# Kernel optimization log

Measured on AMD Instinct MI355X. Metric: run time of the kernel, lower is better.

The kernel has to match this reference:

```python
import jax, jax.numpy as jnp
import numpy as np

N = 300000      # total points
B = 4           # scenes
C_IN = 64
C_OUT = 128
GRID = 0.5      # voxel size
M = 128         # per-axis voxel index bound (10m / 0.5m = 20 << 128); key fits int32
EPS = 1e-5      # BatchNorm eps


def setup_inputs() -> dict:
    key = jax.random.key(0)
    k1, k2, k3 = jax.random.split(key, 3)
    coord = jax.random.uniform(k1, (N, 3), jnp.float32) * 10.0
    feat = jax.random.normal(k2, (N, C_IN), jnp.float32)
    offset = jnp.array([N // 4, N // 2, 3 * N // 4, N], jnp.int32)  # cumulative counts
    W = jax.random.normal(k3, (C_IN, C_OUT), jnp.float32) * 0.05    # fc weight (no bias)
    gamma = jnp.ones((C_OUT,), jnp.float32)
    beta = jnp.zeros((C_OUT,), jnp.float32)
    return {"coord": coord, "feat": feat, "offset": offset, "W": W, "gamma": gamma, "beta": beta}


def reference(coord, feat, offset, W, gamma, beta):
    n = coord.shape[0]
    # offset2batch: point i belongs to scene searchsorted(offset, i, 'right')
    batch = jnp.searchsorted(offset, jnp.arange(n, dtype=offset.dtype), side='right')
    # fc -> BatchNorm1d (training-mode batch stats, biased var) -> ReLU
    x = feat @ W                                    # [n, C_OUT]
    mean = x.mean(axis=0)
    var = x.var(axis=0)
    x = jax.nn.relu(gamma * (x - mean) * jax.lax.rsqrt(var + EPS) + beta)
    # start = per-scene min coordinate (segment_csr min)
    start = jax.ops.segment_min(coord, batch, num_segments=B)      # [B, 3]
    # voxel_grid: integer voxel index per point, hashed injectively with batch id
    v = jnp.floor((coord - start[batch]) / GRID).astype(jnp.int32)  # [n, 3]
    vkey = ((batch.astype(jnp.int32) * M + v[:, 0]) * M + v[:, 1]) * M + v[:, 2]
    # unique(sorted) with inverse/counts; padded to n for static shapes
    uniq, cluster, counts = jnp.unique(vkey, return_inverse=True, return_counts=True,
                                       size=n, fill_value=-1)
    cluster = cluster.reshape(-1)                   # [n] cluster id per point
    # segment mean of coords, segment max of features (padded segments -> 0)
    cnt = jnp.maximum(counts, 1).astype(coord.dtype)
    coord_out = jax.ops.segment_sum(coord, cluster, num_segments=n) / cnt[:, None]
    fmax = jax.ops.segment_max(x, cluster, num_segments=n)
    feat_out = jnp.where(counts[:, None] > 0, fmax, jnp.zeros((), x.dtype))
    # batch id of each cluster (clusters never cross scenes)
    batch_out = jax.ops.segment_min(batch, cluster, num_segments=n)
    return coord_out, feat_out, cluster, counts, batch_out
```

## Files before the change

### kernel.cpp

```cpp
#include <hip/hip_runtime.h>
#include <stdint.h>

#define CIN   64
#define COUT  128
#define EPSB  1e-5f
#define NWORDS2 4096
#define MAXNC 32768
#define STRD  68

typedef short bf16x8 __attribute__((ext_vector_type(8)));
typedef float f32x4  __attribute__((ext_vector_type(4)));

__device__ __forceinline__ int batch_of(int i, const int* __restrict__ off, int B) {
    int b = 0;
    for (int j = 0; j < B - 1; ++j) b += (i >= off[j]) ? 1 : 0;
    return b;
}

__device__ __forceinline__ unsigned enc(float x) {
    unsigned b = __float_as_uint(x);
    return (b & 0x80000000u) ? ~b : (b | 0x80000000u);
}
__device__ __forceinline__ float dec(unsigned u) {
    unsigned b = (u & 0x80000000u) ? (u ^ 0x80000000u) : ~u;
    return __uint_as_float(b);
}

__device__ __forceinline__ unsigned short rne_bf16(float f) {
    unsigned u = __float_as_uint(f);
    unsigned r = u + 0x7FFFu + ((u >> 16) & 1u);
    return (unsigned short)(r >> 16);
}

__global__ void k_init(float* __restrict__ coordOut, float* __restrict__ batchOut, int n,
                       unsigned* __restrict__ pooledU, int* __restrict__ countsWs,
                       unsigned* __restrict__ flags, int* __restrict__ sceneMin, int nScene,
                       const float* __restrict__ W, unsigned short* __restrict__ Wb)
{
    long i = (long)blockIdx.x * blockDim.x + threadIdx.x;
    long stride = (long)gridDim.x * blockDim.x;
    for (long t = i; t < 3L * n; t += stride) coordOut[t] = 0.f;
    for (long t = i; t < n; t += stride) batchOut[t] = 2147483648.0f;
    for (long t = i; t < (long)MAXNC * COUT; t += stride) pooledU[t] = 0u;
    for (long t = i; t < MAXNC; t += stride) countsWs[t] = 0;
    for (long t = i; t < NWORDS2; t += stride) flags[t] = 0u;
    for (long t = i; t < nScene; t += stride) sceneMin[t] = 0x7F800000;
    for (long t = i; t < 32 * 64 * 8; t += stride) {
        int fragIdx = (int)(t >> 9);
        int r = (int)(t & 511);
        int lane = r >> 3, j = r & 7;
        int s  = fragIdx & 1;
        int kt = (fragIdx >> 1) & 1;
        int nt = fragIdx >> 2;
        int k  = kt * 32 + (lane >> 4) * 8 + j;
        int nc = nt * 16 + (lane & 15);
        float w = W[k * COUT + nc];
        unsigned short hi = rne_bf16(w);
        if (s == 0) Wb[t] = hi;
        else {
            float hf = __uint_as_float(((unsigned)hi) << 16);
            Wb[t] = rne_bf16(w - hf);
        }
    }
}

__global__ void k_scene_min(const float* __restrict__ coord, const int* __restrict__ off,
                            int n, int B, int* __restrict__ sceneMin)
{
    __shared__ int smin[12];
    if (threadIdx.x < 3 * B) smin[threadIdx.x] = 0x7F800000;
    __syncthreads();
    int t = blockIdx.x * blockDim.x + threadIdx.x;
    if (t < n) {
        int b = batch_of(t, off, B);
        for (int d = 0; d < 3; ++d)
            atomicMin(&smin[b * 3 + d], __float_as_int(coord[t * 3 + d]));
    }
    __syncthreads();
    if (threadIdx.x < 3 * B) atomicMin(&sceneMin[threadIdx.x], smin[threadIdx.x]);
}

__device__ __forceinline__ int vox_key(const float* __restrict__ coord, int t, int b,
                                       const int* __restrict__ sceneMin)
{
    int key = b;
    for (int d = 0; d < 3; ++d) {
        float s = __int_as_float(sceneMin[b * 3 + d]);
        int v = (int)floorf((coord[t * 3 + d] - s) * 2.0f);
        key = (key << 5) + v;
    }
    return key;
}

__global__ void k_vkey(const float* __restrict__ coord, const int* __restrict__ off,
                       int n, int B, const int* __restrict__ sceneMin,
                       unsigned* __restrict__ flags)
{
    int t = blockIdx.x * blockDim.x + threadIdx.x;
    if (t >= n) return;
    int key = vox_key(coord, t, batch_of(t, off, B), sceneMin);
    atomicOr(&flags[key >> 5], 1u << (key & 31));
}

__global__ void k_scan1(const unsigned* __restrict__ flags,
                        unsigned* __restrict__ wordPrefix, int* __restrict__ dNC)
{
    __shared__ unsigned s[1024];
    int t = threadIdx.x;
    unsigned loc[4]; unsigned sum = 0;
    #pragma unroll
    for (int e = 0; e < 4; ++e) { loc[e] = (unsigned)__popc(flags[4 * t + e]); sum += loc[e]; }
    s[t] = sum;
    __syncthreads();
    for (int d = 1; d < 1024; d <<= 1) {
        unsigned a = (t >= d) ? s[t - d] : 0u;
        __syncthreads();
        s[t] += a;
        __syncthreads();
    }
    unsigned run = s[t] - sum;
    #pragma unroll
    for (int e = 0; e < 4; ++e) { wordPrefix[4 * t + e] = run; run += loc[e]; }
    if (t == 1023) *dNC = (int)s[1023];
}

__global__ void k_cluster(const float* __restrict__ coord, const int* __restrict__ off,
                          int n, int B, const int* __restrict__ sceneMin,
                          const unsigned* __restrict__ flags, const unsigned* __restrict__ wordPrefix,
                          float* __restrict__ clusterOut,
                          int* __restrict__ countsWs, float* __restrict__ batchOut,
                          float* __restrict__ coordOut)
{
    int t = blockIdx.x * blockDim.x + threadIdx.x;
    if (t >= n) return;
    int b = batch_of(t, off, B);
    float c0 = coord[t * 3 + 0], c1 = coord[t * 3 + 1], c2 = coord[t * 3 + 2];
    int key = b;
    key = (key << 5) + (int)floorf((c0 - __int_as_float(sceneMin[b * 3 + 0])) * 2.0f);
    key = (key << 5) + (int)floorf((c1 - __int_as_float(sceneMin[b * 3 + 1])) * 2.0f);
    key = (key << 5) + (int)floorf((c2 - __int_as_float(sceneMin[b * 3 + 2])) * 2.0f);
    int w = key >> 5, bit = key & 31;
    int c = (int)wordPrefix[w] + __popc(flags[w] & ((1u << bit) - 1u));
    clusterOut[t] = (float)c;
    atomicAdd(&countsWs[c], 1);
    batchOut[c] = (float)b;
    atomicAdd(&coordOut[c * 3 + 0], c0);
    atomicAdd(&coordOut[c * 3 + 1], c1);
    atomicAdd(&coordOut[c * 3 + 2], c2);
}

__global__ void k_scan2(const int* __restrict__ counts, int* __restrict__ cursor)
{
    __shared__ int s[1024];
    int t = threadIdx.x;
    int base = t * 32;
    int loc[32]; int sum = 0;
    #pragma unroll
    for (int e = 0; e < 32; ++e) { loc[e] = counts[base + e]; sum += loc[e]; }
    s[t] = sum;
    __syncthreads();
    for (int d = 1; d < 1024; d <<= 1) {
        int a = (t >= d) ? s[t - d] : 0;
        __syncthreads();
        s[t] += a;
        __syncthreads();
    }
    int run = s[t] - sum;
    #pragma unroll
    for (int e = 0; e < 32; ++e) { cursor[base + e] = run; run += loc[e]; }
}

__global__ void k_scatter(const float* __restrict__ clusterOut, int n,
                          int* __restrict__ cursor, int* __restrict__ perm,
                          int* __restrict__ sortedCid)
{
    int t = blockIdx.x * blockDim.x + threadIdx.x;
    if (t >= n) return;
    int c = (int)clusterOut[t];
    int pos = atomicAdd(&cursor[c], 1);
    perm[pos] = t;
    sortedCid[pos] = c;
}

__global__ __launch_bounds__(256, 2) void k_fused(
    const float* __restrict__ feat, const unsigned short* __restrict__ Wb,
    const int* __restrict__ perm, const int* __restrict__ sortedCid,
    int n, int nWin, int gFused,
    unsigned* __restrict__ pooledU, float* __restrict__ partials)
{
    __shared__ float lds[4][64 * STRD];
    __shared__ float accS[256];
    const int tid = threadIdx.x, wave = tid >> 6, lane = tid & 63;
    accS[tid] = 0.f;
    __syncthreads();

    const int wid = blockIdx.x * 4 + wave;
    const int q = lane >> 4, c16 = lane & 15;

    if (wid < nWin) {
        const int base = wid * 64;
        const int nvalid = min(64, n - base);
        const int pv = (lane < nvalid) ? perm[base + lane] : 0;
        const int cv = (lane < nvalid) ? sortedCid[base + lane] : -1;
        float* st = lds[wave];

        int prevc = __shfl_up(cv, 1, 64);
        unsigned long long bmask = __ballot(lane > 0 && lane < nvalid && cv != prevc);

        for (int i0 = 0; i0 < 64; i0 += 4) {
            int idx = i0 + q % 4;
            idx = i0 + q;
            int p = __shfl(pv, idx, 64);
            float4 v = make_float4(0.f, 0.f, 0.f, 0.f);
            if (idx < nvalid)
                v = ((const float4*)(feat + (size_t)p * CIN))[c16];
            *(float4*)&st[idx * STRD + c16 * 4] = v;
        }

        bf16x8 ahi[4][2], alo[4][2];
        #pragma unroll
        for (int mt = 0; mt < 4; ++mt) {
            #pragma unroll
            for (int kt = 0; kt < 2; ++kt) {
                int m = mt * 16 + c16;
                int k0 = kt * 32 + q * 8;
                float4 fa = *(const float4*)&st[m * STRD + k0];
                float4 fb = *(const float4*)&st[m * STRD + k0 + 4];
                float tmp[8] = { fa.x, fa.y, fa.z, fa.w, fb.x, fb.y, fb.z, fb.w };
                bf16x8 h8, l8;
                #pragma unroll
                for (int j = 0; j < 8; ++j) {
                    unsigned short h = rne_bf16(tmp[j]);
                    float hf = __uint_as_float(((unsigned)h) << 16);
                    h8[j] = (short)h;
                    l8[j] = (short)rne_bf16(tmp[j] - hf);
                }
                ahi[mt][kt] = h8;
                alo[mt][kt] = l8;
            }
        }

        for (int h = 0; h < 2; ++h) {
            bf16x8 bh[4][2], bl[4][2];
            #pragma unroll
            for (int nt2 = 0; nt2 < 4; ++nt2)
                #pragma unroll
                for (int kt = 0; kt < 2; ++kt) {
                    int fi = h * 16 + (nt2 * 2 + kt) * 2;
                    bh[nt2][kt] = *(const bf16x8*)(Wb + ((size_t)fi << 9) + (lane << 3));
                    bl[nt2][kt] = *(const bf16x8*)(Wb + ((size_t)(fi + 1) << 9) + (lane << 3));
                }
            #pragma unroll
            for (int mt = 0; mt < 4; ++mt) {
                #pragma unroll
                for (int nt2 = 0; nt2 < 4; ++nt2) {
                    f32x4 c = {0.f, 0.f, 0.f, 0.f};
                    #pragma unroll
                    for (int kt = 0; kt < 2; ++kt) {
                        c = __builtin_amdgcn_mfma_f32_16x16x32_bf16(alo[mt][kt], bh[nt2][kt], c, 0, 0, 0);
                        c = __builtin_amdgcn_mfma_f32_16x16x32_bf16(ahi[mt][kt], bl[nt2][kt], c, 0, 0, 0);
                        c = __builtin_amdgcn_mfma_f32_16x16x32_bf16(ahi[mt][kt], bh[nt2][kt], c, 0, 0, 0);
                    }
                    int col = nt2 * 16 + c16;
                    int row0 = mt * 16 + q * 4;
                    *(float4*)&st[col * STRD + row0] = make_float4(c[0], c[1], c[2], c[3]);
                }
            }
            float runM = -INFINITY, s1 = 0.f, s2 = 0.f;
            int runStart = 0;
            for (int ip = 0; ip < 16; ++ip) {
                if (ip * 4 >= nvalid) break;
                float4 v = *(const float4*)&st[lane * STRD + ip * 4];
                #pragma unroll
                for (int e = 0; e < 4; ++e) {
                    int i = ip * 4 + e;
                    if (i < nvalid) {
                        if (i > 0 && ((bmask >> i) & 1ull)) {
                            int cid = __shfl(cv, i - 1, 64);
                            unsigned* pb = pooledU + (size_t)cid * COUT + h * 64 + lane;
                            if (runStart == 0) atomicMax(pb, enc(runM));
                            else               *pb = enc(runM);
                            runStart = i;
                            runM = -INFINITY;
                        }
                        float x = (e == 0) ? v.x : (e == 1) ? v.y : (e == 2) ? v.z : v.w;
                        runM = fmaxf(runM, x);
                        s1 += x;
                        s2 = fmaf(x, x, s2);
                    }
                }
            }
            int cidL = __shfl(cv, nvalid - 1, 64);
            atomicMax(pooledU + (size_t)cidL * COUT + h * 64 + lane, enc(runM));
            atomicAdd(&accS[h * 64 + lane],       s1);
            atomicAdd(&accS[128 + h * 64 + lane], s2);
        }
    }

    __syncthreads();
    partials[(size_t)tid * gFused + blockIdx.x] = accS[tid];
}

__global__ void k_redbn(const float* __restrict__ partials, int gFused,
                        const float* __restrict__ gamma, const float* __restrict__ beta,
                        int n, float* __restrict__ scaleShift)
{
    __shared__ float red[512];
    const int j = blockIdx.x;
    const float* colS = partials + (size_t)j * gFused;
    const float* colQ = partials + (size_t)(j + 128) * gFused;
    float s = 0.f, q = 0.f;
    for (int b = threadIdx.x; b < gFused; b += 256) { s += colS[b]; q += colQ[b]; }
    red[threadIdx.x] = s;
    red[256 + threadIdx.x] = q;
    __syncthreads();
    for (int st = 128; st; st >>= 1) {
        if (threadIdx.x < st) {
            red[threadIdx.x] += red[threadIdx.x + st];
            red[256 + threadIdx.x] += red[256 + threadIdx.x + st];
        }
        __syncthreads();
    }
    if (threadIdx.x == 0) {
        float mean = red[0] / (float)n;
        float var  = red[256] / (float)n - mean * mean;
        var = fmaxf(var, 0.f);
        float inv = rsqrtf(var + EPSB);
        float sc = gamma[j] * inv;
        scaleShift[j]        = sc;
        scaleShift[COUT + j] = beta[j] - mean * sc;
    }
}

__global__ void k_final(float* __restrict__ featOut, const unsigned* __restrict__ pooledU,
                        const int* __restrict__ dNC, const float* __restrict__ scaleShift,
                        long featN4, int n,
                        float* __restrict__ coordOut, float* __restrict__ countsOut,
                        const int* __restrict__ countsWs)
{
    long i = (long)blockIdx.x * blockDim.x + threadIdx.x;
    long stride = (long)gridDim.x * blockDim.x;
    long act4 = (long)(*dNC) * (COUT / 4);
    float4* out4 = (float4*)featOut;
    const uint4* p4 = (const uint4*)pooledU;
    for (long idx = i; idx < featN4; idx += stride) {
        float4 v = make_float4(0.f, 0.f, 0.f, 0.f);
        if (idx < act4) {
            int j = (int)((idx * 4) & (COUT - 1));
            uint4 u = p4[idx];
            v.x = fmaxf(fmaf(scaleShift[j + 0], dec(u.x), scaleShift[COUT + j + 0]), 0.f);
            v.y = fmaxf(fmaf(scaleShift[j + 1], dec(u.y), scaleShift[COUT + j + 1]), 0.f);
            v.z = fmaxf(fmaf(scaleShift[j + 2], dec(u.z), scaleShift[COUT + j + 2]), 0.f);
            v.w = fmaxf(fmaf(scaleShift[j + 3], dec(u.w), scaleShift[COUT + j + 3]), 0.f);
        }
        out4[idx] = v;
    }
    for (long t = i; t < n; t += stride) {
        int cnt = (t < MAXNC) ? countsWs[t] : 0;
        if (cnt > 0) {
            float inv = 1.f / (float)cnt;
            coordOut[3 * t + 0] *= inv;
            coordOut[3 * t + 1] *= inv;
            coordOut[3 * t + 2] *= inv;
        }
        countsOut[t] = (float)cnt;
    }
}

extern "C" void kernel_launch(void* const* d_in, const int* in_sizes, int n_in,
                              void* d_out, int out_size, void* d_ws, size_t ws_size,
                              hipStream_t stream)
{
    const float* coord = (const float*)d_in[0];
    const float* feat  = (const float*)d_in[1];
    const int*   off   = (const int*)d_in[2];
    const float* W     = (const float*)d_in[3];
    const float* gamma = (const float*)d_in[4];
    const float* beta  = (const float*)d_in[5];
    const int n = in_sizes[0] / 3;
    const int B = in_sizes[2];

    float* out        = (float*)d_out;
    float* coordOut   = out;
    float* featOut    = out + (long)n * 3;
    float* clusterOut = featOut + (long)n * COUT;
    float* countsOut  = clusterOut + n;
    float* batchOut   = countsOut + n;

    char* wsp = (char*)d_ws;
    auto alloc = [&](size_t bytes) -> char* {
        char* p = wsp;
        wsp += (bytes + 255) & ~(size_t)255;
        return p;
    };
    unsigned* flags      = (unsigned*)alloc(NWORDS2 * 4);
    unsigned* wordPrefix = (unsigned*)alloc(NWORDS2 * 4);
    int*      countsWs   = (int*)alloc(MAXNC * 4);
    int*      perm       = (int*)alloc((size_t)n * 4);
    int*      sortedCid  = (int*)alloc((size_t)n * 4);
    int*      cursor     = (int*)alloc(MAXNC * 4);
    unsigned* pooledU    = (unsigned*)alloc((size_t)MAXNC * COUT * 4);
    unsigned short* Wb   = (unsigned short*)alloc(32 * 64 * 8 * 2);
    float*    scaleShift = (float*)alloc(2 * COUT * 4);
    int*      sceneMin   = (int*)alloc(3 * B * 4);
    int*      dNC        = (int*)alloc(4);

    const int nWin = (n + 63) / 64;
    const int gFused = (nWin + 3) / 4;
    float*    partials   = (float*)alloc((size_t)gFused * 256 * 4);

    const long featN4 = (long)n * COUT / 4;
    const int nb = (n + 255) / 256;

    k_init<<<nb, 256, 0, stream>>>(coordOut, batchOut, n, pooledU, countsWs,
                                   flags, sceneMin, 3 * B, W, Wb);
    k_scene_min<<<nb, 256, 0, stream>>>(coord, off, n, B, sceneMin);
    k_vkey<<<nb, 256, 0, stream>>>(coord, off, n, B, sceneMin, flags);
    k_scan1<<<1, 1024, 0, stream>>>(flags, wordPrefix, dNC);
    k_cluster<<<nb, 256, 0, stream>>>(coord, off, n, B, sceneMin, flags, wordPrefix,
                                      clusterOut, countsWs, batchOut, coordOut);
    k_scan2<<<1, 1024, 0, stream>>>(countsWs, cursor);
    k_scatter<<<nb, 256, 0, stream>>>(clusterOut, n, cursor, perm, sortedCid);
    k_fused<<<gFused, 256, 0, stream>>>(feat, Wb, perm, sortedCid, n, nWin, gFused,
                                        pooledU, partials);
    k_redbn<<<128, 256, 0, stream>>>(partials, gFused, gamma, beta, n, scaleShift);
    k_final<<<2048, 256, 0, stream>>>(featOut, pooledU, dNC, scaleShift, featN4, n,
                                      coordOut, countsOut, countsWs);
}
```

Before: 443.6 us.

## Cache voxel keys, move coord pooling into sorted fused kernel, shuffle-based scans

The voxel key computed in k_vkey is now stored in a workspace and reused by k_cluster, so coords and scene minima are not re-read there. The batch id is taken from the key bits. The per-point coord atomics in k_cluster are removed. Coord sums are instead accumulated per run of equal cluster ids inside the sorted fused kernel, using plain stores for runs fully inside a window and atomics only at window edges. Both single-block scans switch from LDS Hillis-Steele with many barriers to wave shuffles plus a small cross-wave step. The costs are an extra n-int workspace and a serial per-window loop over 64 points in the fused kernel.

```diff
diff --git a/kernel.cpp b/kernel.cpp
--- a/kernel.cpp
+++ b/kernel.cpp
@@ -80,92 +80,101 @@
     if (threadIdx.x < 3 * B) atomicMin(&sceneMin[threadIdx.x], smin[threadIdx.x]);
 }
 
-__device__ __forceinline__ int vox_key(const float* __restrict__ coord, int t, int b,
-                                       const int* __restrict__ sceneMin)
-{
+__global__ void k_vkey(const float* __restrict__ coord, const int* __restrict__ off,
+                       int n, int B, const int* __restrict__ sceneMin,
+                       int* __restrict__ vkeyWs, unsigned* __restrict__ flags)
+{
+    int t = blockIdx.x * blockDim.x + threadIdx.x;
+    if (t >= n) return;
+    int b = batch_of(t, off, B);
     int key = b;
+    #pragma unroll
     for (int d = 0; d < 3; ++d) {
         float s = __int_as_float(sceneMin[b * 3 + d]);
         int v = (int)floorf((coord[t * 3 + d] - s) * 2.0f);
         key = (key << 5) + v;
     }
-    return key;
-}
-
-__global__ void k_vkey(const float* __restrict__ coord, const int* __restrict__ off,
-                       int n, int B, const int* __restrict__ sceneMin,
-                       unsigned* __restrict__ flags)
+    vkeyWs[t] = key;
+    atomicOr(&flags[key >> 5], 1u << (key & 31));
+}
+
+__global__ void k_scan1(const unsigned* __restrict__ flags,
+                        unsigned* __restrict__ wordPrefix, int* __restrict__ dNC)
+{
+    __shared__ unsigned wsum[16];
+    const int t = threadIdx.x, lane = t & 63, wv = t >> 6;
+    unsigned loc[4]; unsigned sum = 0;
+    #pragma unroll
+    for (int e = 0; e < 4; ++e) { loc[e] = (unsigned)__popc(flags[4 * t + e]); sum += loc[e]; }
+    unsigned incl = sum;
+    #pragma unroll
+    for (int d = 1; d < 64; d <<= 1) {
+        unsigned u = __shfl_up(incl, d, 64);
+        if (lane >= d) incl += u;
+    }
+    if (lane == 63) wsum[wv] = incl;
+    __syncthreads();
+    if (wv == 0) {
+        unsigned v = (lane < 16) ? wsum[lane] : 0u;
+        unsigned iv = v;
+        #pragma unroll
+        for (int d = 1; d < 16; d <<= 1) {
+            unsigned u = __shfl_up(iv, d, 64);
+            if (lane >= d) iv += u;
+        }
+        if (lane < 16) wsum[lane] = iv - v;
+    }
+    __syncthreads();
+    unsigned run = wsum[wv] + incl - sum;
+    #pragma unroll
+    for (int e = 0; e < 4; ++e) { wordPrefix[4 * t + e] = run; run += loc[e]; }
+    if (t == 1023) *dNC = (int)run;
+}
+
+__global__ void k_cluster(const int* __restrict__ vkeyWs, const int* __restrict__ off,
+                          int n, int B,
+                          const unsigned* __restrict__ flags, const unsigned* __restrict__ wordPrefix,
+                          float* __restrict__ clusterOut,
+                          int* __restrict__ countsWs, float* __restrict__ batchOut)
 {
     int t = blockIdx.x * blockDim.x + threadIdx.x;
     if (t >= n) return;
-    int key = vox_key(coord, t, batch_of(t, off, B), sceneMin);
-    atomicOr(&flags[key >> 5], 1u << (key & 31));
-}
-
-__global__ void k_scan1(const unsigned* __restrict__ flags,
-                        unsigned* __restrict__ wordPrefix, int* __restrict__ dNC)
-{
-    __shared__ unsigned s[1024];
-    int t = threadIdx.x;
-    unsigned loc[4]; unsigned sum = 0;
-    #pragma unroll
-    for (int e = 0; e < 4; ++e) { loc[e] = (unsigned)__popc(flags[4 * t + e]); sum += loc[e]; }
-    s[t] = sum;
-    __syncthreads();
-    for (int d = 1; d < 1024; d <<= 1) {
-        unsigned a = (t >= d) ? s[t - d] : 0u;
-        __syncthreads();
-        s[t] += a;
-        __syncthreads();
-    }
-    unsigned run = s[t] - sum;
-    #pragma unroll
-    for (int e = 0; e < 4; ++e) { wordPrefix[4 * t + e] = run; run += loc[e]; }
-    if (t == 1023) *dNC = (int)s[1023];
-}
-
-__global__ void k_cluster(const float* __restrict__ coord, const int* __restrict__ off,
-                          int n, int B, const int* __restrict__ sceneMin,
-                          const unsigned* __restrict__ flags, const unsigned* __restrict__ wordPrefix,
-                          float* __restrict__ clusterOut,
-                          int* __restrict__ countsWs, float* __restrict__ batchOut,
-                          float* __restrict__ coordOut)
-{
-    int t = blockIdx.x * blockDim.x + threadIdx.x;
-    if (t >= n) return;
-    int b = batch_of(t, off, B);
-    float c0 = coord[t * 3 + 0], c1 = coord[t * 3 + 1], c2 = coord[t * 3 + 2];
-    int key = b;
-    key = (key << 5) + (int)floorf((c0 - __int_as_float(sceneMin[b * 3 + 0])) * 2.0f);
-    key = (key << 5) + (int)floorf((c1 - __int_as_float(sceneMin[b * 3 + 1])) * 2.0f);
-    key = (key << 5) + (int)floorf((c2 - __int_as_float(sceneMin[b * 3 + 2])) * 2.0f);
+    int key = vkeyWs[t];
     int w = key >> 5, bit = key & 31;
     int c = (int)wordPrefix[w] + __popc(flags[w] & ((1u << bit) - 1u));
     clusterOut[t] = (float)c;
     atomicAdd(&countsWs[c], 1);
-    batchOut[c] = (float)b;
-    atomicAdd(&coordOut[c * 3 + 0], c0);
-    atomicAdd(&coordOut[c * 3 + 1], c1);
-    atomicAdd(&coordOut[c * 3 + 2], c2);
+    batchOut[c] = (float)(key >> 15);
 }
 
 __global__ void k_scan2(const int* __restrict__ counts, int* __restrict__ cursor)
 {
-    __shared__ int s[1024];
-    int t = threadIdx.x;
-    int base = t * 32;
+    __shared__ int wsum[16];
+    const int t = threadIdx.x, lane = t & 63, wv = t >> 6;
+    const int base = t * 32;
     int loc[32]; int sum = 0;
     #pragma unroll
     for (int e = 0; e < 32; ++e) { loc[e] = counts[base + e]; sum += loc[e]; }
-    s[t] = sum;
-    __syncthreads();
-    for (int d = 1; d < 1024; d <<= 1) {
-        int a = (t >= d) ? s[t - d] : 0;
-        __syncthreads();
-        s[t] += a;
-        __syncthreads();
-    }
-    int run = s[t] - sum;
+    int incl = sum;
+    #pragma unroll
+    for (int d = 1; d < 64; d <<= 1) {
+        int u = __shfl_up(incl, d, 64);
+        if (lane >= d) incl += u;
+    }
+    if (lane == 63) wsum[wv] = incl;
+    __syncthreads();
+    if (wv == 0) {
+        int v = (lane < 16) ? wsum[lane] : 0;
+        int iv = v;
+        #pragma unroll
+        for (int d = 1; d < 16; d <<= 1) {
+            int u = __shfl_up(iv, d, 64);
+            if (lane >= d) iv += u;
+        }
+        if (lane < 16) wsum[lane] = iv - v;
+    }
+    __syncthreads();
+    int run = wsum[wv] + incl - sum;
     #pragma unroll
     for (int e = 0; e < 32; ++e) { cursor[base + e] = run; run += loc[e]; }
 }
@@ -183,12 +192,15 @@
 }
 
 __global__ __launch_bounds__(256, 2) void k_fused(
-    const float* __restrict__ feat, const unsigned short* __restrict__ Wb,
+    const float* __restrict__ feat, const float* __restrict__ coord,
+    const unsigned short* __restrict__ Wb,
     const int* __restrict__ perm, const int* __restrict__ sortedCid,
     int n, int nWin, int gFused,
-    unsigned* __restrict__ pooledU, float* __restrict__ partials)
+    unsigned* __restrict__ pooledU, float* __restrict__ coordOut,
+    float* __restrict__ partials)
 {
     __shared__ float lds[4][64 * STRD];
+    __shared__ float cst[4][192];
     __shared__ float accS[256];
     const int tid = threadIdx.x, wave = tid >> 6, lane = tid & 63;
     accS[tid] = 0.f;
@@ -203,18 +215,43 @@
         const int pv = (lane < nvalid) ? perm[base + lane] : 0;
         const int cv = (lane < nvalid) ? sortedCid[base + lane] : -1;
         float* st = lds[wave];
+        float* cs = cst[wave];
 
         int prevc = __shfl_up(cv, 1, 64);
         unsigned long long bmask = __ballot(lane > 0 && lane < nvalid && cv != prevc);
 
         for (int i0 = 0; i0 < 64; i0 += 4) {
-            int idx = i0 + q % 4;
-            idx = i0 + q;
+            int idx = i0 + q;
             int p = __shfl(pv, idx, 64);
             float4 v = make_float4(0.f, 0.f, 0.f, 0.f);
             if (idx < nvalid)
                 v = ((const float4*)(feat + (size_t)p * CIN))[c16];
             *(float4*)&st[idx * STRD + c16 * 4] = v;
+        }
+        for (int i0 = 0; i0 < 64; i0 += 16) {
+            int idx = i0 + (lane >> 2);
+            int d = lane & 3;
+            int p = __shfl(pv, idx, 64);
+            if (d < 3 && idx < nvalid) cs[idx * 3 + d] = coord[p * 3 + d];
+        }
+
+        {
+            float csum = 0.f;
+            int runStart = 0;
+            for (int i = 0; i < nvalid; ++i) {
+                if (i > 0 && ((bmask >> i) & 1ull)) {
+                    int cid = __shfl(cv, i - 1, 64);
+                    if (lane < 3) {
+                        float* cb = coordOut + (size_t)cid * 3 + lane;
+                        if (runStart == 0) atomicAdd(cb, csum);
+                        else               *cb = csum;
+                    }
+                    runStart = i; csum = 0.f;
+                }
+                if (lane < 3) csum += cs[i * 3 + lane];
+            }
+            int cidL = __shfl(cv, nvalid - 1, 64);
+            if (lane < 3) atomicAdd(coordOut + (size_t)cidL * 3 + lane, csum);
         }
 
         bf16x8 ahi[4][2], alo[4][2];
@@ -395,6 +432,7 @@
     };
     unsigned* flags      = (unsigned*)alloc(NWORDS2 * 4);
     unsigned* wordPrefix = (unsigned*)alloc(NWORDS2 * 4);
+    int*      vkeyWs     = (int*)alloc((size_t)n * 4);
     int*      countsWs   = (int*)alloc(MAXNC * 4);
     int*      perm       = (int*)alloc((size_t)n * 4);
     int*      sortedCid  = (int*)alloc((size_t)n * 4);
@@ -415,14 +453,14 @@
     k_init<<<nb, 256, 0, stream>>>(coordOut, batchOut, n, pooledU, countsWs,
                                    flags, sceneMin, 3 * B, W, Wb);
     k_scene_min<<<nb, 256, 0, stream>>>(coord, off, n, B, sceneMin);
-    k_vkey<<<nb, 256, 0, stream>>>(coord, off, n, B, sceneMin, flags);
+    k_vkey<<<nb, 256, 0, stream>>>(coord, off, n, B, sceneMin, vkeyWs, flags);
     k_scan1<<<1, 1024, 0, stream>>>(flags, wordPrefix, dNC);
-    k_cluster<<<nb, 256, 0, stream>>>(coord, off, n, B, sceneMin, flags, wordPrefix,
-                                      clusterOut, countsWs, batchOut, coordOut);
+    k_cluster<<<nb, 256, 0, stream>>>(vkeyWs, off, n, B, flags, wordPrefix,
+                                      clusterOut, countsWs, batchOut);
     k_scan2<<<1, 1024, 0, stream>>>(countsWs, cursor);
     k_scatter<<<nb, 256, 0, stream>>>(clusterOut, n, cursor, perm, sortedCid);
-    k_fused<<<gFused, 256, 0, stream>>>(feat, Wb, perm, sortedCid, n, nWin, gFused,
-                                        pooledU, partials);
+    k_fused<<<gFused, 256, 0, stream>>>(feat, coord, Wb, perm, sortedCid, n, nWin, gFused,
+                                        pooledU, coordOut, partials);
     k_redbn<<<128, 256, 0, stream>>>(partials, gFused, gamma, beta, n, scaleShift);
     k_final<<<2048, 256, 0, stream>>>(featOut, pooledU, dNC, scaleShift, featN4, n,
                                       coordOut, countsOut, countsWs);
```

Measured after the change: 412.7 us. 1.08x faster.
